# Kernel optimization log

Hardware: AMD Instinct MI355X
Metric: run time of the kernel (lower is better)

The kernel has to match this reference:

```python
import jax, jax.numpy as jnp
import numpy as np

N_NODES = 100000
IN_C, HID_C, OUT_C = 128, 64, 40
N_EDGES = 1600000


def setup_inputs() -> dict:
    key = jax.random.key(0)
    k1, k2, k3, k4, k5, k6 = jax.random.split(key, 6)
    x = jax.random.normal(k1, (N_NODES, IN_C), dtype=jnp.float32)
    edge_index = jax.random.randint(k2, (2, N_EDGES), 0, N_NODES, dtype=jnp.int32)
    # Glorot-style init for GCN weights, zero bias (as in PyG GCNConv)
    W1 = jax.random.normal(k3, (IN_C, HID_C), dtype=jnp.float32) / np.sqrt(IN_C)
    b1 = jnp.zeros((HID_C,), dtype=jnp.float32)
    W2 = jax.random.normal(k4, (HID_C, OUT_C), dtype=jnp.float32) / np.sqrt(HID_C)
    b2 = jnp.zeros((OUT_C,), dtype=jnp.float32)
    return {"x": x, "edge_index": edge_index, "W1": W1, "b1": b1, "W2": W2, "b2": b2}


def gcn_conv(x, src, dst, W, b, n_nodes):
    # PyG GCNConv: self-loops added, symmetric deg^{-1/2} normalization,
    # linear transform first, then normalized scatter-sum aggregation, then bias.
    deg = jnp.zeros((n_nodes,), dtype=x.dtype).at[dst].add(1.0)
    dinv = jnp.where(deg > 0, jax.lax.rsqrt(deg), 0.0)
    norm = dinv[src] * dinv[dst]                      # [E]
    h = x @ W                                          # [N, out]
    msg = h[src] * norm[:, None]                       # [E, out] (gather)
    out = jax.ops.segment_sum(msg, dst, num_segments=n_nodes)  # scatter-add
    return out + b


def reference(x, edge_index, W1, b1, W2, b2):
    n = x.shape[0]
    loop = jnp.arange(n, dtype=edge_index.dtype)
    src = jnp.concatenate([edge_index[0], loop])
    dst = jnp.concatenate([edge_index[1], loop])
    h = jax.nn.relu(gcn_conv(x, src, dst, W1, b1, n))
    # F.dropout with training=False -> identity (eval mode)
    return gcn_conv(h, src, dst, W2, b2, n)
```

## Files before the change

kernel.cpp:

```cpp
#include <hip/hip_runtime.h>

#define N_NODES 100000
#define IN_C    128
#define HID_C   64
#define OUT_C   40
#define N_EDGES 1600000

#define BSH        8
#define NBUCK      ((N_NODES + 255) >> BSH)
#define CAP        5120
#define PART_CHUNK 4096
#define NPB        ((N_EDGES + PART_CHUNK - 1) / PART_CHUNK)
#define EPT        (PART_CHUNK / 256)

typedef _Float16 half_t;
typedef _Float16 half8   __attribute__((ext_vector_type(8)));
typedef _Float16 half2_t __attribute__((ext_vector_type(2)));
typedef float    f32x4   __attribute__((ext_vector_type(4)));
typedef unsigned long long ull;

static __device__ __forceinline__ void acc8(float* a, uint2 v, float sc) {
    char4 lo = __builtin_bit_cast(char4, v.x);
    char4 hi = __builtin_bit_cast(char4, v.y);
    a[0] += sc * (float)lo.x; a[1] += sc * (float)lo.y;
    a[2] += sc * (float)lo.z; a[3] += sc * (float)lo.w;
    a[4] += sc * (float)hi.x; a[5] += sc * (float)hi.y;
    a[6] += sc * (float)hi.z; a[7] += sc * (float)hi.w;
}

static __device__ __forceinline__ void acc16(float* a, uint4 v, float sc) {
    char4 c0 = __builtin_bit_cast(char4, v.x);
    char4 c1 = __builtin_bit_cast(char4, v.y);
    char4 c2 = __builtin_bit_cast(char4, v.z);
    char4 c3 = __builtin_bit_cast(char4, v.w);
    a[0]  += sc * (float)c0.x; a[1]  += sc * (float)c0.y;
    a[2]  += sc * (float)c0.z; a[3]  += sc * (float)c0.w;
    a[4]  += sc * (float)c1.x; a[5]  += sc * (float)c1.y;
    a[6]  += sc * (float)c1.z; a[7]  += sc * (float)c1.w;
    a[8]  += sc * (float)c2.x; a[9]  += sc * (float)c2.y;
    a[10] += sc * (float)c2.z; a[11] += sc * (float)c2.w;
    a[12] += sc * (float)c3.x; a[13] += sc * (float)c3.y;
    a[14] += sc * (float)c3.z; a[15] += sc * (float)c3.w;
}

__global__ void k_init(const float* __restrict__ W1, const float* __restrict__ W2,
                       half_t* __restrict__ W1T, half_t* __restrict__ W2T,
                       int* __restrict__ gcur) {
    int t = threadIdx.x;
    if (t < NBUCK) gcur[t] = t * CAP;
    for (int i = t; i < IN_C * HID_C; i += 512) {
        int k = i >> 6, n = i & 63;
        W1T[n * IN_C + k] = (half_t)W1[i];
    }
    for (int i = t; i < 48 * HID_C; i += 512) {
        int n = i >> 6, k = i & 63;
        W2T[n * HID_C + k] = (n < OUT_C) ? (half_t)W2[k * OUT_C + n] : (half_t)0.0f;
    }
}

__global__ void k_part(const int* __restrict__ src, const int* __restrict__ dst,
                       int* __restrict__ gcur, int* __restrict__ srcs,
                       unsigned char* __restrict__ d8) {
    __shared__ int lh[NBUCK];
    int tid = threadIdx.x;
    for (int i = tid; i < NBUCK; i += 256) lh[i] = 0;
    __syncthreads();
    int base = blockIdx.x * PART_CHUNK;
    int sv[EPT], dv[EPT], rv[EPT];
#pragma unroll
    for (int j = 0; j < EPT; ++j) {
        int e = base + j * 256 + tid;
        if (e < N_EDGES) {
            sv[j] = src[e];
            dv[j] = dst[e];
            rv[j] = atomicAdd(&lh[dv[j] >> BSH], 1);
        } else {
            dv[j] = -1;
        }
    }
    __syncthreads();
    for (int i = tid; i < NBUCK; i += 256) {
        int c = lh[i];
        if (c) lh[i] = atomicAdd(&gcur[i], c);
    }
    __syncthreads();
#pragma unroll
    for (int j = 0; j < EPT; ++j) {
        if (dv[j] >= 0) {
            int pos = lh[dv[j] >> BSH] + rv[j];
            srcs[pos] = sv[j];
            d8[pos]   = (unsigned char)(dv[j] & 255);
        }
    }
}

__global__ void k_bbuild(const int* __restrict__ srcs, const unsigned char* __restrict__ d8,
                         const int* __restrict__ gcur, int* __restrict__ cursor,
                         int* __restrict__ cnt, float* __restrict__ dinv,
                         int* __restrict__ esrc) {
    __shared__ int lc[256];
    __shared__ int ls[256];
    __shared__ int lcur[256];
    int b = blockIdx.x, tid = threadIdx.x;
    int nbase = b << BSH;
    int s0 = b * CAP, s1 = gcur[b];

    lc[tid] = 0;
    __syncthreads();
    for (int e = s0 + tid; e < s1; e += 256)
        atomicAdd(&lc[d8[e]], 1);
    __syncthreads();

    int v = lc[tid];
    ls[tid] = v;
    __syncthreads();
    for (int off = 1; off < 256; off <<= 1) {
        int t = (tid >= off) ? ls[tid - off] : 0;
        __syncthreads();
        ls[tid] += t;
        __syncthreads();
    }
    int excl = ls[tid] - v;
    int node = nbase + tid;
    int rowstart = s0 + excl;
    lcur[tid] = rowstart;
    if (node < N_NODES) {
        cursor[node] = rowstart;
        cnt[node]    = v;
        dinv[node]   = rsqrtf(1.0f + (float)v);
    }
    __syncthreads();

    for (int e = s0 + tid; e < s1; e += 256) {
        int d = d8[e];
        int s = srcs[e];
        int pos = atomicAdd(&lcur[d], 1);
        esrc[pos] = s;
    }
}

__global__ void k_gemm1_mfma(const float* __restrict__ x, const half_t* __restrict__ W1T,
                             const float* __restrict__ dinv, signed char* __restrict__ g1q,
                             float* __restrict__ scales) {
    __shared__ __align__(16) signed char lq[16 * HID_C];
    int lane = threadIdx.x & 63;
    int l16  = lane & 15;
    int lg   = lane >> 4;

    half8 bf[4][4];
#pragma unroll
    for (int ct = 0; ct < 4; ++ct)
#pragma unroll
        for (int kc = 0; kc < 4; ++kc)
            bf[ct][kc] = *(const half8*)(W1T + (ct * 16 + l16) * IN_C + kc * 32 + lg * 8);

#pragma unroll
    for (int s = 0; s < 2; ++s) {
        int r0 = (blockIdx.x * 2 + s) * 16;
        f32x4 acc0 = {0.f, 0.f, 0.f, 0.f};
        f32x4 acc1 = {0.f, 0.f, 0.f, 0.f};
        f32x4 acc2 = {0.f, 0.f, 0.f, 0.f};
        f32x4 acc3 = {0.f, 0.f, 0.f, 0.f};
#pragma unroll
        for (int kc = 0; kc < 4; ++kc) {
            const float* ap = x + (size_t)(r0 + l16) * IN_C + kc * 32 + lg * 8;
            float4 a0 = *(const float4*)ap;
            float4 a1 = *(const float4*)(ap + 4);
            half8 af;
            af[0] = (_Float16)a0.x; af[1] = (_Float16)a0.y;
            af[2] = (_Float16)a0.z; af[3] = (_Float16)a0.w;
            af[4] = (_Float16)a1.x; af[5] = (_Float16)a1.y;
            af[6] = (_Float16)a1.z; af[7] = (_Float16)a1.w;
            acc0 = __builtin_amdgcn_mfma_f32_16x16x32_f16(af, bf[0][kc], acc0, 0, 0, 0);
            acc1 = __builtin_amdgcn_mfma_f32_16x16x32_f16(af, bf[1][kc], acc1, 0, 0, 0);
            acc2 = __builtin_amdgcn_mfma_f32_16x16x32_f16(af, bf[2][kc], acc2, 0, 0, 0);
            acc3 = __builtin_amdgcn_mfma_f32_16x16x32_f16(af, bf[3][kc], acc3, 0, 0, 0);
        }
#pragma unroll
        for (int j = 0; j < 4; ++j) {
            int   r  = r0 + lg * 4 + j;
            float dv = dinv[r];
            float v0 = acc0[j] * dv;
            float v1 = acc1[j] * dv;
            float v2 = acc2[j] * dv;
            float v3 = acc3[j] * dv;
            float m = fmaxf(fmaxf(fabsf(v0), fabsf(v1)), fmaxf(fabsf(v2), fabsf(v3)));
            m = fmaxf(m, __shfl_xor(m, 1));
            m = fmaxf(m, __shfl_xor(m, 2));
            m = fmaxf(m, __shfl_xor(m, 4));
            m = fmaxf(m, __shfl_xor(m, 8));
            float inv = (m > 0.0f) ? 127.0f / m : 0.0f;
            if (l16 == 0) scales[r] = m * (1.0f / 127.0f);
            int q0 = min(127, max(-127, __float2int_rn(v0 * inv)));
            int q1 = min(127, max(-127, __float2int_rn(v1 * inv)));
            int q2 = min(127, max(-127, __float2int_rn(v2 * inv)));
            int q3 = min(127, max(-127, __float2int_rn(v3 * inv)));
            int rl = lg * 4 + j;
            lq[rl * HID_C +  0 + l16] = (signed char)q0;
            lq[rl * HID_C + 16 + l16] = (signed char)q1;
            lq[rl * HID_C + 32 + l16] = (signed char)q2;
            lq[rl * HID_C + 48 + l16] = (signed char)q3;
        }
        uint4 wv = *(const uint4*)(lq + lane * 16);
        *(uint4*)(g1q + (size_t)r0 * HID_C + lane * 16) = wv;
    }
}

__global__ void k_pull1(const int* __restrict__ cursor, const int* __restrict__ cnt,
                        const int* __restrict__ esrc, const float* __restrict__ dinv,
                        const uint4* __restrict__ g1v, const float* __restrict__ scales,
                        const float* __restrict__ b1, half_t* __restrict__ h1) {
    int w    = threadIdx.x >> 6;
    int lane = threadIdx.x & 63;
    int hl   = lane & 31;
    int hh   = lane >> 5;
    int slot = hl >> 2;
    int c16  = hl & 3;
    int n    = blockIdx.x * 8 + w * 2 + hh;

    float dn  = dinv[n];
    int start = cursor[n];
    int mycnt = cnt[n];

    float a[16];
#pragma unroll
    for (int j = 0; j < 16; ++j) a[j] = 0.f;
    if (slot == 0)
        acc16(a, g1v[(size_t)n * 4 + c16], scales[n]);

    int maxcnt = max(mycnt, __shfl_xor(mycnt, 32));

    int e = 0;
    for (; e + 16 <= maxcnt; e += 16) {
        bool ok0 = (e + slot) < mycnt;
        bool ok1 = (e + 8 + slot) < mycnt;
        int i0 = esrc[ok0 ? (start + e + slot) : start];
        int i1 = esrc[ok1 ? (start + e + 8 + slot) : start];
        i0 = ok0 ? i0 : 0;
        i1 = ok1 ? i1 : 0;
        uint4 v0 = g1v[(size_t)i0 * 4 + c16];
        float s0 = ok0 ? scales[i0] : 0.f;
        uint4 v1 = g1v[(size_t)i1 * 4 + c16];
        float s1 = ok1 ? scales[i1] : 0.f;
        acc16(a, v0, s0);
        acc16(a, v1, s1);
    }
    for (; e < maxcnt; e += 8) {
        bool ok = (e + slot) < mycnt;
        int idx = esrc[ok ? (start + e + slot) : start];
        idx = ok ? idx : 0;
        uint4 v = g1v[(size_t)idx * 4 + c16];
        float s = ok ? scales[idx] : 0.f;
        acc16(a, v, s);
    }

#pragma unroll
    for (int j = 0; j < 16; ++j) {
        a[j] += __shfl_xor(a[j], 4);
        a[j] += __shfl_xor(a[j], 8);
        a[j] += __shfl_xor(a[j], 16);
    }

    if (slot == 0) {
        const float4* bp = (const float4*)(b1 + c16 * 16);
        uint4 u0, u1;
        unsigned us[8];
#pragma unroll
        for (int q = 0; q < 4; ++q) {
            float4 bb = bp[q];
            float r0 = fmaxf(dn * a[q * 4 + 0] + bb.x, 0.f);
            float r1 = fmaxf(dn * a[q * 4 + 1] + bb.y, 0.f);
            float r2 = fmaxf(dn * a[q * 4 + 2] + bb.z, 0.f);
            float r3 = fmaxf(dn * a[q * 4 + 3] + bb.w, 0.f);
            half2_t p0; p0.x = (_Float16)r0; p0.y = (_Float16)r1;
            half2_t p1; p1.x = (_Float16)r2; p1.y = (_Float16)r3;
            us[q * 2 + 0] = __builtin_bit_cast(unsigned, p0);
            us[q * 2 + 1] = __builtin_bit_cast(unsigned, p1);
        }
        u0.x = us[0]; u0.y = us[1]; u0.z = us[2]; u0.w = us[3];
        u1.x = us[4]; u1.y = us[5]; u1.z = us[6]; u1.w = us[7];
        half_t* hp = h1 + (size_t)n * HID_C + c16 * 16;
        *(uint4*)hp = u0;
        *(uint4*)(hp + 8) = u1;
    }
}

__global__ void k_gemm2_mfma(const half_t* __restrict__ h1, const half_t* __restrict__ W2T,
                             const float* __restrict__ dinv, signed char* __restrict__ g2q,
                             float* __restrict__ scales2) {
    __shared__ __align__(16) signed char lq[16 * 40];
    int lane = threadIdx.x & 63;
    int l16  = lane & 15;
    int lg   = lane >> 4;

    half8 bf[3][2];
#pragma unroll
    for (int ct = 0; ct < 3; ++ct)
#pragma unroll
        for (int kc = 0; kc < 2; ++kc)
            bf[ct][kc] = *(const half8*)(W2T + (ct * 16 + l16) * HID_C + kc * 32 + lg * 8);

#pragma unroll
    for (int s = 0; s < 2; ++s) {
        int r0 = (blockIdx.x * 2 + s) * 16;
        f32x4 acc0 = {0.f, 0.f, 0.f, 0.f};
        f32x4 acc1 = {0.f, 0.f, 0.f, 0.f};
        f32x4 acc2 = {0.f, 0.f, 0.f, 0.f};
#pragma unroll
        for (int kc = 0; kc < 2; ++kc) {
            half8 af = *(const half8*)(h1 + (size_t)(r0 + l16) * HID_C + kc * 32 + lg * 8);
            acc0 = __builtin_amdgcn_mfma_f32_16x16x32_f16(af, bf[0][kc], acc0, 0, 0, 0);
            acc1 = __builtin_amdgcn_mfma_f32_16x16x32_f16(af, bf[1][kc], acc1, 0, 0, 0);
            acc2 = __builtin_amdgcn_mfma_f32_16x16x32_f16(af, bf[2][kc], acc2, 0, 0, 0);
        }
#pragma unroll
        for (int j = 0; j < 4; ++j) {
            int   r  = r0 + lg * 4 + j;
            float dv = dinv[r];
            float v0 = acc0[j] * dv;
            float v1 = acc1[j] * dv;
            float v2 = (l16 < 8) ? acc2[j] * dv : 0.0f;
            float m = fmaxf(fmaxf(fabsf(v0), fabsf(v1)), fabsf(v2));
            m = fmaxf(m, __shfl_xor(m, 1));
            m = fmaxf(m, __shfl_xor(m, 2));
            m = fmaxf(m, __shfl_xor(m, 4));
            m = fmaxf(m, __shfl_xor(m, 8));
            float inv = (m > 0.0f) ? 127.0f / m : 0.0f;
            if (l16 == 0) scales2[r] = m * (1.0f / 127.0f);
            int q0 = min(127, max(-127, __float2int_rn(v0 * inv)));
            int q1 = min(127, max(-127, __float2int_rn(v1 * inv)));
            int q2 = min(127, max(-127, __float2int_rn(v2 * inv)));
            int rl = lg * 4 + j;
            lq[rl * 40 +  0 + l16] = (signed char)q0;
            lq[rl * 40 + 16 + l16] = (signed char)q1;
            if (l16 < 8) lq[rl * 40 + 32 + l16] = (signed char)q2;
        }
        if (lane < 40)
            *(uint4*)(g2q + (size_t)r0 * 40 + lane * 16) = *(const uint4*)(lq + lane * 16);
    }
}

__global__ void k_pull2(const int* __restrict__ cursor, const int* __restrict__ cnt,
                        const int* __restrict__ esrc, const float* __restrict__ dinv,
                        const signed char* __restrict__ g2q, const float* __restrict__ scales2,
                        const float* __restrict__ b2, float* __restrict__ out) {
    int w    = threadIdx.x >> 6;
    int lane = threadIdx.x & 63;
    int n    = blockIdx.x * 4 + w;
    int slot = lane >> 3;
    int c8   = lane & 7;

    float dn  = dinv[n];
    int start = cursor[n];
    int end   = start + cnt[n];

    float a[8] = {0.f, 0.f, 0.f, 0.f, 0.f, 0.f, 0.f, 0.f};
    if (slot == 0) {
        uint2 v = *(const uint2*)(g2q + (size_t)n * 40 + c8 * 8);
        acc8(a, v, scales2[n]);
    }

    int e = start;
    for (; e + 16 <= end; e += 16) {
        int i0 = esrc[e + slot];
        int i1 = esrc[e + 8 + slot];
        uint2 v0 = *(const uint2*)(g2q + (size_t)i0 * 40 + c8 * 8);
        float s0 = scales2[i0];
        uint2 v1 = *(const uint2*)(g2q + (size_t)i1 * 40 + c8 * 8);
        float s1 = scales2[i1];
        acc8(a, v0, s0);
        acc8(a, v1, s1);
    }
    for (; e < end; e += 8) {
        int  ee  = e + slot;
        bool ok  = ee < end;
        int  idx = esrc[ok ? ee : end - 1];
        uint2 v = *(const uint2*)(g2q + (size_t)idx * 40 + c8 * 8);
        float s = ok ? scales2[idx] : 0.f;
        acc8(a, v, s);
    }

#pragma unroll
    for (int j = 0; j < 8; ++j) {
        a[j] += __shfl_xor(a[j], 8);
        a[j] += __shfl_xor(a[j], 16);
        a[j] += __shfl_xor(a[j], 32);
    }

    if (slot == 0 && c8 < 5) {
        const float* bp = b2 + c8 * 8;
        float* op = out + (size_t)n * OUT_C + c8 * 8;
        float4 r0, r1;
        r0.x = bp[0] + dn * a[0];
        r0.y = bp[1] + dn * a[1];
        r0.z = bp[2] + dn * a[2];
        r0.w = bp[3] + dn * a[3];
        r1.x = bp[4] + dn * a[4];
        r1.y = bp[5] + dn * a[5];
        r1.z = bp[6] + dn * a[6];
        r1.w = bp[7] + dn * a[7];
        *(float4*)op = r0;
        *(float4*)(op + 4) = r1;
    }
}

extern "C" void kernel_launch(void* const* d_in, const int* in_sizes, int n_in,
                              void* d_out, int out_size, void* d_ws, size_t ws_size,
                              hipStream_t stream) {
    const float* x   = (const float*)d_in[0];
    const int*   ei  = (const int*)d_in[1];
    const int*   src = ei;
    const int*   dst = ei + N_EDGES;
    const float* W1  = (const float*)d_in[2];
    const float* b1  = (const float*)d_in[3];
    const float* W2  = (const float*)d_in[4];
    const float* b2  = (const float*)d_in[5];
    float*       out = (float*)d_out;

    const int SLAB = NBUCK * CAP;
    int*    cnt    = (int*)d_ws;
    int*    cursor = cnt + N_NODES;
    int*    gcur   = cursor + N_NODES;
    half_t* w1t    = (half_t*)(gcur + 512);
    half_t* w2t    = w1t + IN_C * HID_C;
    float*  dinv   = (float*)(w2t + 48 * HID_C);
    float*  scales = dinv + N_NODES;
    float*  scales2= scales + N_NODES;
    int*    srcs   = (int*)(scales2 + N_NODES);
    int*    esrc   = srcs + SLAB + 8;
    unsigned char* d8 = (unsigned char*)(esrc + SLAB + 8);
    signed char* g1q = (signed char*)(((uintptr_t)(d8 + SLAB) + 127) & ~(uintptr_t)127);
    half_t* h1 = (half_t*)(g1q + (size_t)N_NODES * 64);
    signed char* g2q = (signed char*)(h1 + (size_t)N_NODES * HID_C);

    k_init<<<1, 512, 0, stream>>>(W1, W2, w1t, w2t, gcur);
    k_part<<<NPB, 256, 0, stream>>>(src, dst, gcur, srcs, d8);
    k_bbuild<<<NBUCK, 256, 0, stream>>>(srcs, d8, gcur, cursor, cnt, dinv, esrc);

    k_gemm1_mfma<<<N_NODES / 32, 64, 0, stream>>>(x, w1t, dinv, g1q, scales);

    k_pull1<<<N_NODES / 8, 256, 0, stream>>>(cursor, cnt, esrc, dinv,
                                             (const uint4*)g1q, scales, b1, h1);

    k_gemm2_mfma<<<N_NODES / 32, 64, 0, stream>>>(h1, w2t, dinv, g2q, scales2);

    k_pull2<<<N_NODES / 4, 256, 0, stream>>>(cursor, cnt, esrc, dinv,
                                             g2q, scales2, b2, out);
}
```

Baseline: 164.2 us.

## Pad layer-2 int8 features to 64 bytes and pull two nodes per wavefront

The int8 layer-2 feature rows go from a 40-byte to a 64-byte stride, zero-padded in shared memory, so the second aggregation can gather with aligned 16-byte loads. k_pull2 now handles two destination nodes per wavefront, each using 32 lanes (8 edge slots by 4 column chunks), with edge loops masked to the larger of the two degrees. The intent is fewer, wider gather transactions and better lane use per node. In exchange, g2q reads move 60% more bytes per row, and lanes sit idle when the two nodes' degrees differ. The padded g2q buffer is 6.4 MB; its placement in the workspace was not changed, which may or may not fit.

```diff
diff --git a/kernel.cpp b/kernel.cpp
--- a/kernel.cpp
+++ b/kernel.cpp
@@ -18,15 +18,6 @@
 typedef _Float16 half2_t __attribute__((ext_vector_type(2)));
 typedef float    f32x4   __attribute__((ext_vector_type(4)));
 typedef unsigned long long ull;
-
-static __device__ __forceinline__ void acc8(float* a, uint2 v, float sc) {
-    char4 lo = __builtin_bit_cast(char4, v.x);
-    char4 hi = __builtin_bit_cast(char4, v.y);
-    a[0] += sc * (float)lo.x; a[1] += sc * (float)lo.y;
-    a[2] += sc * (float)lo.z; a[3] += sc * (float)lo.w;
-    a[4] += sc * (float)hi.x; a[5] += sc * (float)hi.y;
-    a[6] += sc * (float)hi.z; a[7] += sc * (float)hi.w;
-}
 
 static __device__ __forceinline__ void acc16(float* a, uint4 v, float sc) {
     char4 c0 = __builtin_bit_cast(char4, v.x);
@@ -288,7 +279,7 @@
 __global__ void k_gemm2_mfma(const half_t* __restrict__ h1, const half_t* __restrict__ W2T,
                              const float* __restrict__ dinv, signed char* __restrict__ g2q,
                              float* __restrict__ scales2) {
-    __shared__ __align__(16) signed char lq[16 * 40];
+    __shared__ __align__(16) signed char lq[16 * 64];
     int lane = threadIdx.x & 63;
     int l16  = lane & 15;
     int lg   = lane >> 4;
@@ -303,6 +294,7 @@
 #pragma unroll
     for (int s = 0; s < 2; ++s) {
         int r0 = (blockIdx.x * 2 + s) * 16;
+        ((uint4*)lq)[lane] = uint4{0u, 0u, 0u, 0u};
         f32x4 acc0 = {0.f, 0.f, 0.f, 0.f};
         f32x4 acc1 = {0.f, 0.f, 0.f, 0.f};
         f32x4 acc2 = {0.f, 0.f, 0.f, 0.f};
@@ -331,76 +323,84 @@
             int q1 = min(127, max(-127, __float2int_rn(v1 * inv)));
             int q2 = min(127, max(-127, __float2int_rn(v2 * inv)));
             int rl = lg * 4 + j;
-            lq[rl * 40 +  0 + l16] = (signed char)q0;
-            lq[rl * 40 + 16 + l16] = (signed char)q1;
-            if (l16 < 8) lq[rl * 40 + 32 + l16] = (signed char)q2;
-        }
-        if (lane < 40)
-            *(uint4*)(g2q + (size_t)r0 * 40 + lane * 16) = *(const uint4*)(lq + lane * 16);
+            lq[rl * 64 +  0 + l16] = (signed char)q0;
+            lq[rl * 64 + 16 + l16] = (signed char)q1;
+            if (l16 < 8) lq[rl * 64 + 32 + l16] = (signed char)q2;
+        }
+        *(uint4*)(g2q + (size_t)r0 * 64 + lane * 16) = ((const uint4*)lq)[lane];
     }
 }
 
 __global__ void k_pull2(const int* __restrict__ cursor, const int* __restrict__ cnt,
                         const int* __restrict__ esrc, const float* __restrict__ dinv,
-                        const signed char* __restrict__ g2q, const float* __restrict__ scales2,
+                        const uint4* __restrict__ g2v, const float* __restrict__ scales2,
                         const float* __restrict__ b2, float* __restrict__ out) {
     int w    = threadIdx.x >> 6;
     int lane = threadIdx.x & 63;
-    int n    = blockIdx.x * 4 + w;
-    int slot = lane >> 3;
-    int c8   = lane & 7;
+    int hl   = lane & 31;
+    int hh   = lane >> 5;
+    int slot = hl >> 2;
+    int c16  = hl & 3;
+    int n    = blockIdx.x * 8 + w * 2 + hh;
 
     float dn  = dinv[n];
     int start = cursor[n];
-    int end   = start + cnt[n];
-
-    float a[8] = {0.f, 0.f, 0.f, 0.f, 0.f, 0.f, 0.f, 0.f};
-    if (slot == 0) {
-        uint2 v = *(const uint2*)(g2q + (size_t)n * 40 + c8 * 8);
-        acc8(a, v, scales2[n]);
-    }
-
-    int e = start;
-    for (; e + 16 <= end; e += 16) {
-        int i0 = esrc[e + slot];
-        int i1 = esrc[e + 8 + slot];
-        uint2 v0 = *(const uint2*)(g2q + (size_t)i0 * 40 + c8 * 8);
-        float s0 = scales2[i0];
-        uint2 v1 = *(const uint2*)(g2q + (size_t)i1 * 40 + c8 * 8);
-        float s1 = scales2[i1];
-        acc8(a, v0, s0);
-        acc8(a, v1, s1);
-    }
-    for (; e < end; e += 8) {
-        int  ee  = e + slot;
-        bool ok  = ee < end;
-        int  idx = esrc[ok ? ee : end - 1];
-        uint2 v = *(const uint2*)(g2q + (size_t)idx * 40 + c8 * 8);
+    int mycnt = cnt[n];
+
+    float a[16];
+#pragma unroll
+    for (int j = 0; j < 16; ++j) a[j] = 0.f;
+    if (slot == 0)
+        acc16(a, g2v[(size_t)n * 4 + c16], scales2[n]);
+
+    int maxcnt = max(mycnt, __shfl_xor(mycnt, 32));
+
+    int e = 0;
+    for (; e + 16 <= maxcnt; e += 16) {
+        bool ok0 = (e + slot) < mycnt;
+        bool ok1 = (e + 8 + slot) < mycnt;
+        int i0 = esrc[ok0 ? (start + e + slot) : start];
+        int i1 = esrc[ok1 ? (start + e + 8 + slot) : start];
+        i0 = ok0 ? i0 : 0;
+        i1 = ok1 ? i1 : 0;
+        uint4 v0 = g2v[(size_t)i0 * 4 + c16];
+        float s0 = ok0 ? scales2[i0] : 0.f;
+        uint4 v1 = g2v[(size_t)i1 * 4 + c16];
+        float s1 = ok1 ? scales2[i1] : 0.f;
+        acc16(a, v0, s0);
+        acc16(a, v1, s1);
+    }
+    for (; e < maxcnt; e += 8) {
+        bool ok = (e + slot) < mycnt;
+        int idx = esrc[ok ? (start + e + slot) : start];
+        idx = ok ? idx : 0;
+        uint4 v = g2v[(size_t)idx * 4 + c16];
         float s = ok ? scales2[idx] : 0.f;
-        acc8(a, v, s);
-    }
-
-#pragma unroll
-    for (int j = 0; j < 8; ++j) {
+        acc16(a, v, s);
+    }
+
+#pragma unroll
+    for (int j = 0; j < 16; ++j) {
+        a[j] += __shfl_xor(a[j], 4);
         a[j] += __shfl_xor(a[j], 8);
         a[j] += __shfl_xor(a[j], 16);
-        a[j] += __shfl_xor(a[j], 32);
-    }
-
-    if (slot == 0 && c8 < 5) {
-        const float* bp = b2 + c8 * 8;
-        float* op = out + (size_t)n * OUT_C + c8 * 8;
-        float4 r0, r1;
-        r0.x = bp[0] + dn * a[0];
-        r0.y = bp[1] + dn * a[1];
-        r0.z = bp[2] + dn * a[2];
-        r0.w = bp[3] + dn * a[3];
-        r1.x = bp[4] + dn * a[4];
-        r1.y = bp[5] + dn * a[5];
-        r1.z = bp[6] + dn * a[6];
-        r1.w = bp[7] + dn * a[7];
-        *(float4*)op = r0;
-        *(float4*)(op + 4) = r1;
+    }
+
+    if (slot == 0 && c16 < 3) {
+        int nvalid = (c16 < 2) ? 16 : 8;
+        const float* bp = b2 + c16 * 16;
+        float* op = out + (size_t)n * OUT_C + c16 * 16;
+#pragma unroll
+        for (int q = 0; q < 4; ++q) {
+            if (q * 4 < nvalid) {
+                float4 r;
+                r.x = bp[q * 4 + 0] + dn * a[q * 4 + 0];
+                r.y = bp[q * 4 + 1] + dn * a[q * 4 + 1];
+                r.z = bp[q * 4 + 2] + dn * a[q * 4 + 2];
+                r.w = bp[q * 4 + 3] + dn * a[q * 4 + 3];
+                ((float4*)op)[q] = r;
+            }
+        }
     }
 }
 
@@ -444,6 +444,6 @@
 
     k_gemm2_mfma<<<N_NODES / 32, 64, 0, stream>>>(h1, w2t, dinv, g2q, scales2);
 
-    k_pull2<<<N_NODES / 4, 256, 0, stream>>>(cursor, cnt, esrc, dinv,
-                                             g2q, scales2, b2, out);
-}
+    k_pull2<<<N_NODES / 8, 256, 0, stream>>>(cursor, cnt, esrc, dinv,
+                                             (const uint4*)g2q, scales2, b2, out);
+}
```

Measured after the change: 158.8 us, median of 2. -3.3%, faster.
